# Kernel optimization log

Hardware: AMD Instinct MI355X
Metric: run time of the kernel (lower is better)

## Reference

```python
import jax, jax.numpy as jnp
import numpy as np

B, S, D = 4, 1024, 1024
H = 16
HD = D // H  # 64
LN_EPS = 1e-5


def setup_inputs() -> dict:
    key = jax.random.key(0)
    ks = jax.random.split(key, 12)
    s = 1.0 / np.sqrt(D)
    return {
        "x": jax.random.normal(ks[0], (B, S, D), dtype=jnp.float32),
        "wq": jax.random.normal(ks[1], (D, D), dtype=jnp.float32) * s,
        "bq": jnp.zeros((D,), dtype=jnp.float32),
        "wk": jax.random.normal(ks[2], (D, D), dtype=jnp.float32) * s,
        "bk": jnp.zeros((D,), dtype=jnp.float32),
        "wv": jax.random.normal(ks[3], (D, D), dtype=jnp.float32) * s,
        "bv": jnp.zeros((D,), dtype=jnp.float32),
        "wl": jax.random.normal(ks[4], (D, D), dtype=jnp.float32) * s,
        "bl": jnp.zeros((D,), dtype=jnp.float32),
        "ln_g": jnp.ones((D,), dtype=jnp.float32),
        "ln_b": jnp.zeros((D,), dtype=jnp.float32),
    }


def _heads(t):
    # [B,S,D] -> [B,H,S,HD]
    return t.reshape(B, S, H, HD).transpose(0, 2, 1, 3)


def reference(x, wq, bq, wk, bk, wv, bv, wl, bl, ln_g, ln_b):
    q = _heads(x @ wq.T + bq)
    k = _heads(x @ wk.T + bk)
    v = _heads(x @ wv.T + bv)
    score = jnp.einsum("bhqd,bhkd->bhqk", q, k)
    # NOTE: unusual order — softmax first, THEN divide by sqrt(head_size)
    score = jax.nn.softmax(score, axis=-1) / jnp.sqrt(jnp.float32(HD))
    att = jnp.einsum("bhqk,bhkd->bhqd", score, v)
    att = att.transpose(0, 2, 1, 3).reshape(B, S, D)
    # residual added BEFORE the output linear
    y = (att + x) @ wl.T + bl
    # LayerNorm over last dim
    mu = jnp.mean(y, axis=-1, keepdims=True)
    var = jnp.mean(jnp.square(y - mu), axis=-1, keepdims=True)
    out = (y - mu) * jax.lax.rsqrt(var + LN_EPS) * ln_g + ln_b
    # dropout is identity in eval mode
    return out
```

## Files before the change

### kernel.cpp

```cpp
#include <hip/hip_runtime.h>
#include <cstdint>
#include <cstddef>

typedef __bf16 bf16;
typedef __bf16 bf16x4_t __attribute__((ext_vector_type(4)));
typedef __bf16 bf16x8_t __attribute__((ext_vector_type(8)));
typedef float f32x4_t __attribute__((ext_vector_type(4)));

#define DEV static __device__ __forceinline__

DEV void gload16(const void* g, void* l) {
  __builtin_amdgcn_global_load_lds((const __attribute__((address_space(1))) void*)g,
                                   (__attribute__((address_space(3))) void*)l, 16, 0, 0);
}

DEV f32x4_t mfma16(bf16x8_t a, bf16x8_t b, f32x4_t c) {
  return __builtin_amdgcn_mfma_f32_16x16x32_bf16(a, b, c, 0, 0, 0);
}

#define BAR __builtin_amdgcn_s_barrier()
#define FENCE asm volatile("" ::: "memory")
#define VMC(n) asm volatile("s_waitcnt vmcnt(" #n ")" ::: "memory")

__global__ __launch_bounds__(256) void k_convert(
    const float* __restrict__ x, const float* __restrict__ wq,
    const float* __restrict__ wk, const float* __restrict__ wv,
    const float* __restrict__ wl,
    bf16* __restrict__ xb, bf16* __restrict__ wqkvb, bf16* __restrict__ wlb) {
  const size_t M1 = (size_t)1 << 20;
  size_t i = ((size_t)blockIdx.x * 256 + threadIdx.x) * 4;
  const float* src; bf16* dst; size_t off;
  if (i < 4 * M1)      { src = x;  dst = xb;           off = i; }
  else if (i < 5 * M1) { src = wq; dst = wqkvb;        off = i - 4 * M1; }
  else if (i < 6 * M1) { src = wk; dst = wqkvb + M1;   off = i - 5 * M1; }
  else if (i < 7 * M1) { src = wv; dst = wqkvb + 2*M1; off = i - 6 * M1; }
  else                 { src = wl; dst = wlb;          off = i - 7 * M1; }
  f32x4_t v = *(const f32x4_t*)&src[off];
  bf16x4_t o;
  o[0] = (bf16)v[0]; o[1] = (bf16)v[1]; o[2] = (bf16)v[2]; o[3] = (bf16)v[3];
  *(bf16x4_t*)&dst[off] = o;
}

__global__ __launch_bounds__(256) void k_gemm_qkv(
    const bf16* __restrict__ W, const bf16* __restrict__ Xb,
    const float* __restrict__ bq, const float* __restrict__ bk,
    const float* __restrict__ bv,
    bf16* __restrict__ Q, bf16* __restrict__ Kc, bf16* __restrict__ VT) {
  __shared__ alignas(16) bf16 smem[16384];
  bf16* lA = smem;
  bf16* lB = smem + 8192;
  const int tid = threadIdx.x, wave = tid >> 6, lane = tid & 63;
  const int wm = (wave >> 1) * 64, wn = (wave & 1) * 64;
  const int fr = lane & 15, fg = lane >> 4;
  const int csw = (((lane & 7) ^ (lane >> 3)) << 3);
  const int m0 = blockIdx.x * 128, n0 = blockIdx.y * 128;

  f32x4_t acc[4][4];
  const f32x4_t vzero = {0.f, 0.f, 0.f, 0.f};
#pragma unroll
  for (int a = 0; a < 4; ++a)
#pragma unroll
    for (int c = 0; c < 4; ++c) acc[a][c] = vzero;

  const int rowoff = wave * 8 + (lane >> 3);

  for (int kt = 0; kt < 16; ++kt) {
#pragma unroll
    for (int i = 0; i < 4; ++i) {
      gload16(W + (size_t)(m0 + i * 32 + rowoff) * 1024 + kt * 64 + csw,
              &lA[(i * 32 + wave * 8) * 64]);
      gload16(Xb + (size_t)(n0 + i * 32 + rowoff) * 1024 + kt * 64 + csw,
              &lB[(i * 32 + wave * 8) * 64]);
    }
    __syncthreads();
    bf16x8_t af[4][2], bfr[4][2];
#pragma unroll
    for (int mi = 0; mi < 4; ++mi)
#pragma unroll
      for (int ks = 0; ks < 2; ++ks) {
        const int r = wm + mi * 16 + fr;
        af[mi][ks] = *(const bf16x8_t*)
            &lA[r * 64 + ((((ks << 2) + fg) ^ (fr & 7)) << 3)];
      }
#pragma unroll
    for (int ni = 0; ni < 4; ++ni)
#pragma unroll
      for (int ks = 0; ks < 2; ++ks) {
        const int r = wn + ni * 16 + fr;
        bfr[ni][ks] = *(const bf16x8_t*)
            &lB[r * 64 + ((((ks << 2) + fg) ^ (fr & 7)) << 3)];
      }
    __builtin_amdgcn_s_setprio(1);
#pragma unroll
    for (int ks = 0; ks < 2; ++ks)
#pragma unroll
      for (int mi = 0; mi < 4; ++mi)
#pragma unroll
        for (int ni = 0; ni < 4; ++ni)
          acc[mi][ni] = mfma16(af[mi][ks], bfr[ni][ks], acc[mi][ni]);
    __builtin_amdgcn_s_setprio(0);
    __syncthreads();
  }

  const int region = m0 >> 10;
  const float* bp = (region == 0) ? bq : ((region == 1) ? bk : bv);
  if (region < 2) {
    bf16* QK = (region == 0) ? Q : Kc;
#pragma unroll
    for (int mi = 0; mi < 4; ++mi) {
      const int f = (m0 & 1023) + wm + mi * 16 + fg * 4;
      const int h = f >> 6, d = f & 63;
#pragma unroll
      for (int ni = 0; ni < 4; ++ni) {
        const int t = n0 + wn + ni * 16 + fr;
        const int b = t >> 10, s = t & 1023;
        const int bh = b * 16 + h;
        f32x4_t v = acc[mi][ni];
        bf16x4_t o;
#pragma unroll
        for (int j = 0; j < 4; ++j) o[j] = (bf16)(v[j] + bp[f + j]);
        *(bf16x4_t*)&QK[((size_t)bh * 1024 + s) * 64 + d] = o;
      }
    }
  } else {
#pragma unroll
    for (int mi = 0; mi < 4; ++mi) {
      const int dl = wm + mi * 16 + fg * 4;
      const int floc = (m0 & 1023) + dl;
#pragma unroll
      for (int ni = 0; ni < 4; ++ni) {
        const int sl = wn + ni * 16 + fr;
        f32x4_t v = acc[mi][ni];
#pragma unroll
        for (int j = 0; j < 4; ++j) {
          const int d = dl + j;
          smem[d * 128 + (sl ^ ((d & 7) << 3))] = (bf16)(v[j] + bp[floc + j]);
        }
      }
    }
    __syncthreads();
    const int b = n0 >> 10;
#pragma unroll
    for (int i = 0; i < 8; ++i) {
      const int d = i * 16 + (tid >> 4);
      const int c = tid & 15;
      bf16x8_t vv = *(const bf16x8_t*)&smem[d * 128 + ((c ^ (d & 7)) << 3)];
      const int floc = (m0 & 1023) + d;
      const int h = floc >> 6, dd = floc & 63;
      const int sg = (n0 & 1023) + c * 8;
      *(bf16x8_t*)&VT[((size_t)(b * 16 + h) * 64 + dd) * 1024 + sg] = vv;
    }
  }
}

DEV void gemm_mainloop(const bf16* __restrict__ A, const bf16* __restrict__ B,
                       int m0, int n0,
                       bf16 (*lA)[128 * 64], bf16 (*lB)[128 * 64],
                       f32x4_t (&acc)[4][4]) {
  const int tid = threadIdx.x, wave = tid >> 6, lane = tid & 63;
  const int wm = (wave >> 1) * 64, wn = (wave & 1) * 64;
  const int fr = lane & 15, fg = lane >> 4;
  const int rowoff = wave * 8 + (lane >> 3);
  const int csw = (((lane & 7) ^ (lane >> 3)) << 3);

  auto STAGE = [&](int buf, int kt) {
#pragma unroll
    for (int i = 0; i < 4; ++i) {
      gload16(A + (size_t)(m0 + i * 32 + rowoff) * 1024 + kt * 64 + csw,
              &lA[buf][(i * 32 + wave * 8) * 64]);
      gload16(B + (size_t)(n0 + i * 32 + rowoff) * 1024 + kt * 64 + csw,
              &lB[buf][(i * 32 + wave * 8) * 64]);
    }
  };

  auto COMPUTE = [&](int buf) {
    bf16x8_t af[4][2], bfr[4][2];
#pragma unroll
    for (int mi = 0; mi < 4; ++mi)
#pragma unroll
      for (int ks = 0; ks < 2; ++ks) {
        const int r = wm + mi * 16 + fr;
        af[mi][ks] = *(const bf16x8_t*)
            &lA[buf][r * 64 + ((((ks << 2) + fg) ^ (fr & 7)) << 3)];
      }
#pragma unroll
    for (int ni = 0; ni < 4; ++ni)
#pragma unroll
      for (int ks = 0; ks < 2; ++ks) {
        const int r = wn + ni * 16 + fr;
        bfr[ni][ks] = *(const bf16x8_t*)
            &lB[buf][r * 64 + ((((ks << 2) + fg) ^ (fr & 7)) << 3)];
      }
    __builtin_amdgcn_s_setprio(1);
#pragma unroll
    for (int ks = 0; ks < 2; ++ks)
#pragma unroll
      for (int mi = 0; mi < 4; ++mi)
#pragma unroll
        for (int ni = 0; ni < 4; ++ni)
          acc[mi][ni] = mfma16(af[mi][ks], bfr[ni][ks], acc[mi][ni]);
    __builtin_amdgcn_s_setprio(0);
  };

  STAGE(0, 0);
  STAGE(1, 1);
  for (int t = 0; t < 15; ++t) {
    asm volatile("s_waitcnt vmcnt(8)" ::: "memory");
    __builtin_amdgcn_s_barrier();
    COMPUTE(t & 1);
    __builtin_amdgcn_s_barrier();
    if (t < 14) STAGE(t & 1, t + 2);
  }
  asm volatile("s_waitcnt vmcnt(0)" ::: "memory");
  __builtin_amdgcn_s_barrier();
  COMPUTE(1);
}

__global__ __launch_bounds__(256) void k_attn(
    const bf16* __restrict__ Q, const bf16* __restrict__ K,
    const bf16* __restrict__ VT, const float* __restrict__ X,
    bf16* __restrict__ ATTB) {
  __shared__ alignas(16) bf16 lK[2][64 * 64];
  __shared__ alignas(16) bf16 lV[2][64 * 64];
  const int tid = threadIdx.x, wave = tid >> 6, lane = tid & 63;
  const int bh = blockIdx.x, qt = blockIdx.y;
  const int q0 = qt * 128 + wave * 32;
  const int fr = lane & 15, fg = lane >> 4;
  const int rx = (fr & 7) << 3;
  const f32x4_t vzero = {0.f, 0.f, 0.f, 0.f};

  bf16x8_t qf[2][2];
#pragma unroll
  for (int qi = 0; qi < 2; ++qi)
#pragma unroll
    for (int ks = 0; ks < 2; ++ks)
      qf[qi][ks] = *(const bf16x8_t*)
          &Q[((size_t)bh * 1024 + q0 + qi * 16 + fr) * 64 + ks * 32 + fg * 8];

  f32x4_t oacc[2][4];
  float lsum[2] = {0.f, 0.f};
#pragma unroll
  for (int qi = 0; qi < 2; ++qi)
#pragma unroll
    for (int dj = 0; dj < 4; ++dj) oacc[qi][dj] = vzero;

  const int srow = lane >> 3;
  const int scolsw = (((lane & 7) ^ srow) * 8);

  auto STAGE = [&](int buf, int kv) {
#pragma unroll
    for (int i = 0; i < 2; ++i) {
      const int c = wave * 2 + i;
      gload16(&K[((size_t)bh * 1024 + kv * 64 + c * 8 + srow) * 64 + scolsw],
              &lK[buf][c * 512]);
      gload16(&VT[((size_t)bh * 64 + c * 8 + srow) * 1024 + kv * 64 + scolsw],
              &lV[buf][c * 512]);
    }
  };

  auto TILE = [&](int cur) {
    bf16x8_t kb[4][2];
#pragma unroll
    for (int kj = 0; kj < 4; ++kj)
#pragma unroll
      for (int ks = 0; ks < 2; ++ks) {
        const int r = kj * 16 + fr;
        kb[kj][ks] = *(const bf16x8_t*)&lK[cur][r * 64 + ((ks * 32 + fg * 8) ^ rx)];
      }
    f32x4_t s[2][4];
#pragma unroll
    for (int qi = 0; qi < 2; ++qi)
#pragma unroll
      for (int kj = 0; kj < 4; ++kj) {
        f32x4_t z = vzero;
#pragma unroll
        for (int ks = 0; ks < 2; ++ks) z = mfma16(kb[kj][ks], qf[qi][ks], z);
        s[qi][kj] = z;
      }

    bf16x8_t vb[4][2];
#pragma unroll
    for (int dj = 0; dj < 4; ++dj)
#pragma unroll
      for (int ks = 0; ks < 2; ++ks) {
        const int r = dj * 16 + fr;
        const int c0 = ks * 32 + fg * 4;
        const int e0 = (c0 & 7) | ((((c0 >> 3) ^ (r & 7))) << 3);
        const int c1 = c0 + 16;
        const int e1 = (c1 & 7) | ((((c1 >> 3) ^ (r & 7))) << 3);
        bf16x4_t lo = *(const bf16x4_t*)&lV[cur][r * 64 + e0];
        bf16x4_t hi = *(const bf16x4_t*)&lV[cur][r * 64 + e1];
        bf16x8_t vv;
#pragma unroll
        for (int j = 0; j < 4; ++j) { vv[j] = lo[j]; vv[4 + j] = hi[j]; }
        vb[dj][ks] = vv;
      }

    bf16x8_t paf[2][2];
#pragma unroll
    for (int qi = 0; qi < 2; ++qi)
#pragma unroll
      for (int ks = 0; ks < 2; ++ks) {
        bf16x8_t pv;
#pragma unroll
        for (int h = 0; h < 2; ++h)
#pragma unroll
          for (int j = 0; j < 4; ++j) {
            bf16 pb = (bf16)__expf(s[qi][2 * ks + h][j]);
            lsum[qi] += (float)pb;
            pv[h * 4 + j] = pb;
          }
        paf[qi][ks] = pv;
      }

#pragma unroll
    for (int qi = 0; qi < 2; ++qi)
#pragma unroll
      for (int dj = 0; dj < 4; ++dj)
#pragma unroll
        for (int ks = 0; ks < 2; ++ks)
          oacc[qi][dj] = mfma16(paf[qi][ks], vb[dj][ks], oacc[qi][dj]);
  };

  STAGE(0, 0);
  STAGE(1, 1);
  for (int kv = 0; kv < 15; ++kv) {
    VMC(4); BAR; FENCE;
    TILE(kv & 1);
    BAR; FENCE;
    if (kv < 14) STAGE(kv & 1, kv + 2);
  }
  VMC(0); BAR; FENCE;
  TILE(1);

#pragma unroll
  for (int qi = 0; qi < 2; ++qi) {
    lsum[qi] += __shfl_xor(lsum[qi], 16);
    lsum[qi] += __shfl_xor(lsum[qi], 32);
  }
  float rs[2][4];
#pragma unroll
  for (int qi = 0; qi < 2; ++qi)
#pragma unroll
    for (int j = 0; j < 4; ++j)
      rs[qi][j] = __shfl(lsum[qi], fg * 4 + j);

  const int b = bh >> 4, h = bh & 15;
#pragma unroll
  for (int qi = 0; qi < 2; ++qi)
#pragma unroll
    for (int dj = 0; dj < 4; ++dj)
#pragma unroll
      for (int j = 0; j < 4; ++j) {
        const int s_ = q0 + qi * 16 + fg * 4 + j;
        const int d_ = dj * 16 + fr;
        const size_t tok = (size_t)b * 1024 + s_;
        const size_t fidx = (size_t)h * 64 + d_;
        float val = oacc[qi][dj][j] / rs[qi][j] * 0.125f + X[tok * 1024 + fidx];
        ATTB[tok * 1024 + fidx] = (bf16)val;
      }
}

__global__ __launch_bounds__(256, 2) void k_gemm_out(
    const bf16* __restrict__ Wl, const bf16* __restrict__ Ax,
    const float* __restrict__ bl, bf16* __restrict__ Y) {
  __shared__ alignas(16) bf16 lA[2][128 * 64];
  __shared__ alignas(16) bf16 lB[2][128 * 64];
  const f32x4_t vzero = {0.f, 0.f, 0.f, 0.f};
  f32x4_t acc[4][4];
#pragma unroll
  for (int a = 0; a < 4; ++a)
#pragma unroll
    for (int c = 0; c < 4; ++c) acc[a][c] = vzero;
  const int m0 = blockIdx.x * 128, n0 = blockIdx.y * 128;
  gemm_mainloop(Wl, Ax, m0, n0, lA, lB, acc);

  const int tid = threadIdx.x, wave = tid >> 6, lane = tid & 63;
  const int wm = (wave >> 1) * 64, wn = (wave & 1) * 64;
  const int fr = lane & 15, fg = lane >> 4;
#pragma unroll
  for (int mi = 0; mi < 4; ++mi) {
    const int f = m0 + wm + mi * 16 + fg * 4;
#pragma unroll
    for (int ni = 0; ni < 4; ++ni) {
      const int t = n0 + wn + ni * 16 + fr;
      f32x4_t v = acc[mi][ni];
      bf16x4_t o;
#pragma unroll
      for (int j = 0; j < 4; ++j) o[j] = (bf16)(v[j] + bl[f + j]);
      *(bf16x4_t*)&Y[(size_t)t * 1024 + f] = o;
    }
  }
}

__global__ __launch_bounds__(256) void k_ln(
    const bf16* __restrict__ Y, const float* __restrict__ g,
    const float* __restrict__ bta, float* __restrict__ OUT) {
  const int row = blockIdx.x, tid = threadIdx.x;
  const bf16* y = Y + (size_t)row * 1024;
  bf16x4_t yv = *(const bf16x4_t*)&y[tid * 4];
  f32x4_t v;
#pragma unroll
  for (int j = 0; j < 4; ++j) v[j] = (float)yv[j];
  float s = v[0] + v[1] + v[2] + v[3];
  float s2 = v[0]*v[0] + v[1]*v[1] + v[2]*v[2] + v[3]*v[3];
#pragma unroll
  for (int m = 1; m < 64; m <<= 1) {
    s += __shfl_xor(s, m);
    s2 += __shfl_xor(s2, m);
  }
  __shared__ float ps[4], ps2[4];
  const int wave = tid >> 6, lane = tid & 63;
  if (lane == 0) { ps[wave] = s; ps2[wave] = s2; }
  __syncthreads();
  s = ps[0] + ps[1] + ps[2] + ps[3];
  s2 = ps2[0] + ps2[1] + ps2[2] + ps2[3];
  const float mu = s * (1.f / 1024.f);
  const float var = s2 * (1.f / 1024.f) - mu * mu;
  const float rs = rsqrtf(var + 1e-5f);
  f32x4_t gg = *(const f32x4_t*)&g[tid * 4];
  f32x4_t bb = *(const f32x4_t*)&bta[tid * 4];
  f32x4_t o;
#pragma unroll
  for (int j = 0; j < 4; ++j) o[j] = (v[j] - mu) * rs * gg[j] + bb[j];
  *(f32x4_t*)&OUT[(size_t)row * 1024 + tid * 4] = o;
}

extern "C" void kernel_launch(void* const* d_in, const int* in_sizes, int n_in,
                              void* d_out, int out_size, void* d_ws, size_t ws_size,
                              hipStream_t stream) {
  (void)in_sizes; (void)n_in; (void)out_size; (void)ws_size;
  const float* x   = (const float*)d_in[0];
  const float* wq  = (const float*)d_in[1];
  const float* bq  = (const float*)d_in[2];
  const float* wk  = (const float*)d_in[3];
  const float* bk  = (const float*)d_in[4];
  const float* wv  = (const float*)d_in[5];
  const float* bv  = (const float*)d_in[6];
  const float* wl  = (const float*)d_in[7];
  const float* bl  = (const float*)d_in[8];
  const float* lng = (const float*)d_in[9];
  const float* lnb = (const float*)d_in[10];

  const size_t MB = (size_t)1 << 20;
  char* ws = (char*)d_ws;
  bf16* xb    = (bf16*)(ws);
  bf16* wqkvb = (bf16*)(ws + 8 * MB);
  bf16* wlb   = (bf16*)(ws + 14 * MB);
  bf16* Qb    = (bf16*)(ws + 16 * MB);
  bf16* Kb    = (bf16*)(ws + 24 * MB);
  bf16* VTb   = (bf16*)(ws + 32 * MB);
  bf16* attb  = (bf16*)(ws + 40 * MB);
  bf16* Y     = (bf16*)(ws + 16 * MB);

  k_convert<<<dim3(8192), dim3(256), 0, stream>>>(x, wq, wk, wv, wl, xb, wqkvb, wlb);
  k_gemm_qkv<<<dim3(24, 32), dim3(256), 0, stream>>>(wqkvb, xb, bq, bk, bv, Qb, Kb, VTb);
  k_attn<<<dim3(64, 8), dim3(256), 0, stream>>>(Qb, Kb, VTb, x, attb);
  k_gemm_out<<<dim3(8, 32), dim3(256), 0, stream>>>(wlb, attb, bl, Y);
  k_ln<<<dim3(4096), dim3(256), 0, stream>>>(Y, lng, lnb, (float*)d_out);
}
```

Baseline: 109.1 us.

## Stage attention output through LDS for coalesced residual add and store

The attention epilogue now writes the normalized output tile into a swizzled, per-wave region of shared memory. It then reads it back row-wise, so the residual X loads (16-byte float4) and the ATTB stores (16-byte bf16x8) are coalesced, replacing the earlier scattered scalar global accesses. To make this possible, the K/V double buffers are merged into one shared array that the epilogue reuses. Row sums are also accumulated per element in vector registers and reduced only at the end. The trade-off is an extra barrier and an LDS round trip, and the output is rounded to bf16 before the residual add, which adds a small precision change.

```diff
diff --git a/kernel.cpp b/kernel.cpp
--- a/kernel.cpp
+++ b/kernel.cpp
@@ -220,8 +220,7 @@
     const bf16* __restrict__ Q, const bf16* __restrict__ K,
     const bf16* __restrict__ VT, const float* __restrict__ X,
     bf16* __restrict__ ATTB) {
-  __shared__ alignas(16) bf16 lK[2][64 * 64];
-  __shared__ alignas(16) bf16 lV[2][64 * 64];
+  __shared__ alignas(16) bf16 sm[16384];
   const int tid = threadIdx.x, wave = tid >> 6, lane = tid & 63;
   const int bh = blockIdx.x, qt = blockIdx.y;
   const int q0 = qt * 128 + wave * 32;
@@ -238,7 +237,7 @@
           &Q[((size_t)bh * 1024 + q0 + qi * 16 + fr) * 64 + ks * 32 + fg * 8];
 
   f32x4_t oacc[2][4];
-  float lsum[2] = {0.f, 0.f};
+  f32x4_t lsum4[2] = {vzero, vzero};
 #pragma unroll
   for (int qi = 0; qi < 2; ++qi)
 #pragma unroll
@@ -248,24 +247,28 @@
   const int scolsw = (((lane & 7) ^ srow) * 8);
 
   auto STAGE = [&](int buf, int kv) {
+    bf16* dK = sm + buf * 4096;
+    bf16* dV = sm + 8192 + buf * 4096;
 #pragma unroll
     for (int i = 0; i < 2; ++i) {
       const int c = wave * 2 + i;
       gload16(&K[((size_t)bh * 1024 + kv * 64 + c * 8 + srow) * 64 + scolsw],
-              &lK[buf][c * 512]);
+              &dK[c * 512]);
       gload16(&VT[((size_t)bh * 64 + c * 8 + srow) * 1024 + kv * 64 + scolsw],
-              &lV[buf][c * 512]);
+              &dV[c * 512]);
     }
   };
 
   auto TILE = [&](int cur) {
+    const bf16* sK = sm + cur * 4096;
+    const bf16* sV = sm + 8192 + cur * 4096;
     bf16x8_t kb[4][2];
 #pragma unroll
     for (int kj = 0; kj < 4; ++kj)
 #pragma unroll
       for (int ks = 0; ks < 2; ++ks) {
         const int r = kj * 16 + fr;
-        kb[kj][ks] = *(const bf16x8_t*)&lK[cur][r * 64 + ((ks * 32 + fg * 8) ^ rx)];
+        kb[kj][ks] = *(const bf16x8_t*)&sK[r * 64 + ((ks * 32 + fg * 8) ^ rx)];
       }
     f32x4_t s[2][4];
 #pragma unroll
@@ -288,8 +291,8 @@
         const int e0 = (c0 & 7) | ((((c0 >> 3) ^ (r & 7))) << 3);
         const int c1 = c0 + 16;
         const int e1 = (c1 & 7) | ((((c1 >> 3) ^ (r & 7))) << 3);
-        bf16x4_t lo = *(const bf16x4_t*)&lV[cur][r * 64 + e0];
-        bf16x4_t hi = *(const bf16x4_t*)&lV[cur][r * 64 + e1];
+        bf16x4_t lo = *(const bf16x4_t*)&sV[r * 64 + e0];
+        bf16x4_t hi = *(const bf16x4_t*)&sV[r * 64 + e1];
         bf16x8_t vv;
 #pragma unroll
         for (int j = 0; j < 4; ++j) { vv[j] = lo[j]; vv[4 + j] = hi[j]; }
@@ -303,12 +306,12 @@
       for (int ks = 0; ks < 2; ++ks) {
         bf16x8_t pv;
 #pragma unroll
-        for (int h = 0; h < 2; ++h)
+        for (int h2 = 0; h2 < 2; ++h2)
 #pragma unroll
           for (int j = 0; j < 4; ++j) {
-            bf16 pb = (bf16)__expf(s[qi][2 * ks + h][j]);
-            lsum[qi] += (float)pb;
-            pv[h * 4 + j] = pb;
+            bf16 pb = (bf16)__expf(s[qi][2 * ks + h2][j]);
+            lsum4[qi][j] += (float)pb;
+            pv[h2 * 4 + j] = pb;
           }
         paf[qi][ks] = pv;
       }
@@ -333,8 +336,10 @@
   VMC(0); BAR; FENCE;
   TILE(1);
 
+  float lsum[2];
 #pragma unroll
   for (int qi = 0; qi < 2; ++qi) {
+    lsum[qi] = (lsum4[qi][0] + lsum4[qi][1]) + (lsum4[qi][2] + lsum4[qi][3]);
     lsum[qi] += __shfl_xor(lsum[qi], 16);
     lsum[qi] += __shfl_xor(lsum[qi], 32);
   }
@@ -345,20 +350,37 @@
     for (int j = 0; j < 4; ++j)
       rs[qi][j] = __shfl(lsum[qi], fg * 4 + j);
 
+  BAR;
+  bf16* lT = sm + wave * 2048;
+#pragma unroll
+  for (int qi = 0; qi < 2; ++qi)
+#pragma unroll
+    for (int dj = 0; dj < 4; ++dj)
+#pragma unroll
+      for (int j = 0; j < 4; ++j) {
+        const int m = qi * 16 + fg * 4 + j;
+        const int d = dj * 16 + fr;
+        lT[m * 64 + (d ^ ((m & 7) << 3))] =
+            (bf16)(oacc[qi][dj][j] / rs[qi][j] * 0.125f);
+      }
   const int b = bh >> 4, h = bh & 15;
 #pragma unroll
-  for (int qi = 0; qi < 2; ++qi)
-#pragma unroll
-    for (int dj = 0; dj < 4; ++dj)
-#pragma unroll
-      for (int j = 0; j < 4; ++j) {
-        const int s_ = q0 + qi * 16 + fg * 4 + j;
-        const int d_ = dj * 16 + fr;
-        const size_t tok = (size_t)b * 1024 + s_;
-        const size_t fidx = (size_t)h * 64 + d_;
-        float val = oacc[qi][dj][j] / rs[qi][j] * 0.125f + X[tok * 1024 + fidx];
-        ATTB[tok * 1024 + fidx] = (bf16)val;
-      }
+  for (int i = 0; i < 4; ++i) {
+    const int row = i * 8 + (lane >> 3);
+    const int col = (lane & 7) * 8;
+    bf16x8_t av = *(const bf16x8_t*)&lT[row * 64 + (col ^ ((row & 7) << 3))];
+    const size_t tok = (size_t)b * 1024 + q0 + row;
+    const size_t fx = (size_t)h * 64 + col;
+    f32x4_t x0 = *(const f32x4_t*)&X[tok * 1024 + fx];
+    f32x4_t x1 = *(const f32x4_t*)&X[tok * 1024 + fx + 4];
+    bf16x8_t o;
+#pragma unroll
+    for (int j = 0; j < 4; ++j) {
+      o[j] = (bf16)((float)av[j] + x0[j]);
+      o[4 + j] = (bf16)((float)av[4 + j] + x1[j]);
+    }
+    *(bf16x8_t*)&ATTB[tok * 1024 + fx] = o;
+  }
 }
 
 __global__ __launch_bounds__(256, 2) void k_gemm_out(
```

Result: no change. 109.8 us (+0.6%).
